# Performance work log

Hardware: AMD Instinct MI355X
Metric: run time of the kernel (lower is better)

## Reference

```python
import jax, jax.numpy as jnp
import numpy as np
import math

IN_C = 1024
OUT_C = 1024
HEADS = 16
GROUPS = 4

def grouped_linear(src, weight, bias):
    # src: [..., in_c]; weight: [g, in_c//g, out_c//g]; bias: [out_c]
    g, icg, ocg = weight.shape
    lead = src.shape[:-1]
    s = src.reshape(*lead, g, icg)
    out = jnp.einsum('...gi,gio->...go', s, weight)
    out = out.reshape(*lead, g * ocg)
    return out + bias

def restricted_softmax(src, margin=0.0):
    src_max = jnp.maximum(jnp.max(src, axis=-1, keepdims=True), 0.0)
    out = jnp.exp(src - src_max)
    return out / (jnp.sum(out, axis=-1, keepdims=True) + jnp.exp(margin - src_max))

def setup_inputs() -> dict:
    key = jax.random.key(0)
    ks = jax.random.split(key, 9)
    B, S = 2, 2048
    icg, ocg = IN_C // GROUPS, OUT_C // GROUPS
    scale = 1.0 / math.sqrt(icg)
    return {
        'query': jax.random.normal(ks[0], (B, S, IN_C), jnp.float32),
        'key': jax.random.normal(ks[1], (B, S, IN_C), jnp.float32),
        'value': jax.random.normal(ks[2], (B, S, IN_C), jnp.float32),
        'wq': jax.random.uniform(ks[3], (GROUPS, icg, ocg), jnp.float32, -scale, scale),
        'wk': jax.random.uniform(ks[4], (GROUPS, icg, ocg), jnp.float32, -scale, scale),
        'wv': jax.random.uniform(ks[5], (GROUPS, icg, ocg), jnp.float32, -scale, scale),
        'bq': jax.random.uniform(ks[6], (OUT_C,), jnp.float32, -scale, scale),
        'bk': jax.random.uniform(ks[7], (OUT_C,), jnp.float32, -scale, scale),
        'bv': jax.random.uniform(ks[8], (OUT_C,), jnp.float32, -scale, scale),
    }

def reference(query, key, value, wq, wk, wv, bq, bk, bv):
    q = grouped_linear(query, wq, bq)   # [B,S,OUT_C]
    k = grouped_linear(key, wk, bk)
    v = grouped_linear(value, wv, bv)
    B, Sq, _ = q.shape
    Sk = k.shape[-2]
    d = OUT_C // HEADS
    q = q.reshape(B, Sq, HEADS, d).transpose(0, 2, 1, 3)  # [B,H,Sq,d]
    k = k.reshape(B, Sk, HEADS, d).transpose(0, 2, 1, 3)
    v = v.reshape(B, Sk, HEADS, d).transpose(0, 2, 1, 3)
    score = jnp.einsum('bhqd,bhkd->bhqk', q, k) / math.sqrt(d)
    attn = restricted_softmax(score)
    out = jnp.einsum('bhqk,bhkd->bhqd', attn, v)
    out = out.transpose(0, 2, 1, 3).reshape(B, Sq, OUT_C)
    return out
```

## Files before the change

kernel.cpp:

```cpp
#include <hip/hip_runtime.h>
#include <hip/hip_bf16.h>

#define BB 2
#define SS 2048
#define CC 1024
#define HH 16
#define DDIM 64
#define NROWS (BB*SS)

#define QSC 0.18033688011112042f

typedef __attribute__((ext_vector_type(8))) short bf16x8;
typedef __attribute__((ext_vector_type(4))) float f32x4;

__device__ __forceinline__ f32x4 mfma16(bf16x8 a, bf16x8 b, f32x4 c) {
    return __builtin_amdgcn_mfma_f32_16x16x32_bf16(a, b, c, 0, 0, 0);
}

__global__ __launch_bounds__(256) void prep_wt(
    const float* __restrict__ wq, const float* __restrict__ wk,
    const float* __restrict__ wv, __hip_bfloat16* __restrict__ wt)
{
    const float* w = blockIdx.z == 0 ? wq : blockIdx.z == 1 ? wk : wv;
    const int g  = blockIdx.y;
    const int kt = blockIdx.x >> 2;
    const int nt = blockIdx.x & 3;
    __shared__ __hip_bfloat16 Ls[64][72];
    const int t = threadIdx.x;
    #pragma unroll
    for (int j = 0; j < 4; ++j) {
        int f4 = t + j*256;
        int row = f4 >> 4, n0 = (f4 & 15) * 4;
        float4 f = *(const float4*)&w[(size_t)g*65536 + (size_t)(kt*64+row)*256
                                      + nt*64 + n0];
        Ls[n0+0][row] = __float2bfloat16(f.x);
        Ls[n0+1][row] = __float2bfloat16(f.y);
        Ls[n0+2][row] = __float2bfloat16(f.z);
        Ls[n0+3][row] = __float2bfloat16(f.w);
    }
    __syncthreads();
    #pragma unroll
    for (int j = 0; j < 2; ++j) {
        int u = t + j*256;
        int nr = u >> 3, k8 = (u & 7) * 8;
        *(uint4*)&wt[((size_t)(blockIdx.z*4 + g)*256 + nt*64 + nr)*256
                     + kt*64 + k8] = *(const uint4*)&Ls[nr][k8];
    }
}

__global__ __launch_bounds__(256, 3) void proj_mfma(
    const float* __restrict__ qin, const float* __restrict__ kin,
    const float* __restrict__ vin,
    const __hip_bfloat16* __restrict__ wt,
    const float* __restrict__ bq, const float* __restrict__ bk,
    const float* __restrict__ bv,
    __hip_bfloat16* __restrict__ qs, __hip_bfloat16* __restrict__ ks_,
    __hip_bfloat16* __restrict__ vs)
{
    const int z = blockIdx.z;
    const float* src; const float* bias;
    if (z == 0)      { src = qin; bias = bq; }
    else if (z == 1) { src = kin; bias = bk; }
    else             { src = vin; bias = bv; }

    const int hp   = blockIdx.y;
    const int g    = hp >> 1;
    const int col0 = (hp & 1) * 128;
    const int row0 = blockIdx.x * 128;
    const int b    = row0 >> 11;
    const int s0   = row0 & 2047;

    __shared__ char smem[36864];
    auto As = (__hip_bfloat16 (*)[72])smem;
    auto Ws = (__hip_bfloat16 (*)[72])(smem + 18432);

    const int t    = threadIdx.x;
    const int wid  = t >> 6;
    const int lane = t & 63;
    const int l16  = lane & 15;
    const int quad = lane >> 4;

    f32x4 acc[2][8];
    #pragma unroll
    for (int mt = 0; mt < 2; ++mt)
        #pragma unroll
        for (int nt = 0; nt < 8; ++nt) acc[mt][nt] = (f32x4){0.f,0.f,0.f,0.f};

    const __hip_bfloat16* wtz = wt + (size_t)(z*4 + g)*65536;

    for (int kt = 0; kt < 4; ++kt) {
        __syncthreads();
        #pragma unroll
        for (int j = 0; j < 8; ++j) {
            int idx = t + j*256;
            int row = idx >> 4, c4 = (idx & 15) * 4;
            float4 f = *(const float4*)&src[(size_t)(row0 + row)*CC + g*256
                                            + kt*64 + c4];
            union { __hip_bfloat16 hh[4]; uint2 u; } pk;
            pk.hh[0] = __float2bfloat16(f.x); pk.hh[1] = __float2bfloat16(f.y);
            pk.hh[2] = __float2bfloat16(f.z); pk.hh[3] = __float2bfloat16(f.w);
            *(uint2*)&As[row][c4] = pk.u;
        }
        #pragma unroll
        for (int j = 0; j < 4; ++j) {
            int idx = t + j*256;
            int n = idx >> 3, k8 = (idx & 7) * 8;
            *(uint4*)&Ws[n][k8] =
                *(const uint4*)&wtz[(size_t)(col0 + n)*256 + kt*64 + k8];
        }
        __syncthreads();
        #pragma unroll
        for (int kss = 0; kss < 2; ++kss) {
            bf16x8 af[2], wf[8];
            #pragma unroll
            for (int mt = 0; mt < 2; ++mt)
                af[mt] = *(const bf16x8*)&As[wid*32 + mt*16 + l16][kss*32 + quad*8];
            #pragma unroll
            for (int nt = 0; nt < 8; ++nt)
                wf[nt] = *(const bf16x8*)&Ws[nt*16 + l16][kss*32 + quad*8];
            #pragma unroll
            for (int mt = 0; mt < 2; ++mt)
                #pragma unroll
                for (int nt = 0; nt < 8; ++nt)
                    acc[mt][nt] = mfma16(af[mt], wf[nt], acc[mt][nt]);
        }
    }

    float bval[8];
    #pragma unroll
    for (int nt = 0; nt < 8; ++nt) bval[nt] = bias[g*256 + col0 + nt*16 + l16];

    __syncthreads();

    if (z < 2) {
        const float scale = (z == 0) ? QSC : 1.0f;
        auto Ot = (__hip_bfloat16 (*)[136])smem;
        #pragma unroll
        for (int mt = 0; mt < 2; ++mt)
            #pragma unroll
            for (int nt = 0; nt < 8; ++nt)
                #pragma unroll
                for (int r = 0; r < 4; ++r)
                    Ot[wid*32 + mt*16 + quad*4 + r][nt*16 + l16] =
                        __float2bfloat16((acc[mt][nt][r] + bval[nt]) * scale);
        __syncthreads();
        __hip_bfloat16* base = (z == 0) ? qs : ks_;
        #pragma unroll
        for (int j = 0; j < 8; ++j) {
            int f = wid + j*4;
            int hl = f >> 4, t16l = (f >> 1) & 7, kcs = f & 1;
            uint4 v = *(const uint4*)&Ot[t16l*16 + l16][hl*64 + kcs*32 + quad*8];
            int h = hp*2 + hl;
            int t16g = (s0 >> 4) + t16l;
            *(uint4*)&base[((size_t)(b*HH + h) << 17)
                           + ((size_t)(t16g*2 + kcs) << 9) + lane*8] = v;
        }
    } else {
        auto Vl = (__hip_bfloat16 (*)[136])smem;
        #pragma unroll
        for (int mt = 0; mt < 2; ++mt)
            #pragma unroll
            for (int nt = 0; nt < 8; ++nt) {
                union { __hip_bfloat16 hh[4]; uint2 u; } pk;
                #pragma unroll
                for (int r = 0; r < 4; ++r)
                    pk.hh[r] = __float2bfloat16(acc[mt][nt][r] + bval[nt]);
                *(uint2*)&Vl[nt*16 + l16][wid*32 + mt*16 + quad*4] = pk.u;
            }
        __syncthreads();
        const int kc0 = s0 >> 5;
        #pragma unroll
        for (int j = 0; j < 8; ++j) {
            int f = wid + j*4;
            int hl = f >> 4, dt = (f >> 2) & 3, kcl = f & 3;
            uint4 v = *(const uint4*)&Vl[hl*64 + dt*16 + l16][kcl*32 + quad*8];
            int h = hp*2 + hl;
            *(uint4*)&vs[((size_t)(b*HH + h) << 17)
                         + ((size_t)(dt*64 + kc0 + kcl) << 9) + lane*8] = v;
        }
    }
}

__global__ __launch_bounds__(256, 2) void attn_mfma(
    const __hip_bfloat16* __restrict__ qs, const __hip_bfloat16* __restrict__ ks_,
    const __hip_bfloat16* __restrict__ vs, float* __restrict__ out)
{
    const int d   = blockIdx.x;
    const int xcd = d & 7;
    const int s   = d >> 3;
    const int qt  = s & 31;
    const int bh  = (s >> 5) * 8 + xcd;
    const int h   = bh & 15;
    const int b   = bh >> 4;

    __shared__ char smem[37376];
    auto Ps = (__hip_bfloat16 (*)[64][72])smem;
    auto Ub = (float (*)[64][68])smem;
    float* Lb = (float*)(smem + 36864);

    const int t    = threadIdx.x;
    const int wid  = t >> 6;
    const int lane = t & 63;
    const int l16  = lane & 15;
    const int quad = lane >> 4;

    const __hip_bfloat16* qb = qs  + ((size_t)bh << 17);
    const __hip_bfloat16* kb = ks_ + ((size_t)bh << 17);
    const __hip_bfloat16* vb = vs  + ((size_t)bh << 17);

    const bf16x8 onesv = (bf16x8){16256,16256,16256,16256,
                                  16256,16256,16256,16256};

    bf16x8 qf[4][2];
    #pragma unroll
    for (int mt = 0; mt < 4; ++mt)
        #pragma unroll
        for (int kss = 0; kss < 2; ++kss)
            qf[mt][kss] = *(const bf16x8*)(qb +
                ((size_t)((qt*4 + mt)*2 + kss) << 9) + lane*8);

    f32x4 O[4][4];
    f32x4 Lfrag[4];
    #pragma unroll
    for (int mt = 0; mt < 4; ++mt) {
        Lfrag[mt] = (f32x4){0.f,0.f,0.f,0.f};
        #pragma unroll
        for (int dt = 0; dt < 4; ++dt) O[mt][dt] = (f32x4){0.f,0.f,0.f,0.f};
    }

    bf16x8 kf[4][2];
    #pragma unroll
    for (int nt = 0; nt < 4; ++nt)
        #pragma unroll
        for (int kss = 0; kss < 2; ++kss)
            kf[nt][kss] = *(const bf16x8*)(kb +
                ((size_t)((wid*32 + nt)*2 + kss) << 9) + lane*8);

    for (int kt = 0; kt < 8; ++kt) {
        bf16x8 vf[4][2];
        #pragma unroll
        for (int dt = 0; dt < 4; ++dt)
            #pragma unroll
            for (int kss = 0; kss < 2; ++kss)
                vf[dt][kss] = *(const bf16x8*)(vb +
                    ((size_t)(dt*64 + wid*16 + kt*2 + kss) << 9) + lane*8);

        #pragma unroll
        for (int nt = 0; nt < 4; ++nt) {
            f32x4 st[4];
            #pragma unroll
            for (int mt = 0; mt < 4; ++mt) {
                f32x4 z = (f32x4){0.f,0.f,0.f,0.f};
                z = mfma16(kf[nt][0], qf[mt][0], z);
                st[mt] = mfma16(kf[nt][1], qf[mt][1], z);
            }
            #pragma unroll
            for (int mt = 0; mt < 4; ++mt) {
                float2 e0, e1;
                e0.x = __builtin_amdgcn_exp2f(st[mt][0]);
                e0.y = __builtin_amdgcn_exp2f(st[mt][1]);
                e1.x = __builtin_amdgcn_exp2f(st[mt][2]);
                e1.y = __builtin_amdgcn_exp2f(st[mt][3]);
                union { __hip_bfloat162 h2[2]; uint2 u; } pk;
                pk.h2[0] = __float22bfloat162_rn(e0);
                pk.h2[1] = __float22bfloat162_rn(e1);
                *(uint2*)&Ps[wid][mt*16 + l16][nt*16 + quad*4] = pk.u;
            }
        }

        if (kt + 1 < 8) {
            #pragma unroll
            for (int nt = 0; nt < 4; ++nt)
                #pragma unroll
                for (int kss = 0; kss < 2; ++kss)
                    kf[nt][kss] = *(const bf16x8*)(kb +
                        ((size_t)((wid*32 + (kt+1)*4 + nt)*2 + kss) << 9) + lane*8);
        }

        #pragma unroll
        for (int kss = 0; kss < 2; ++kss) {
            bf16x8 pf[4];
            #pragma unroll
            for (int mt = 0; mt < 4; ++mt)
                pf[mt] = *(const bf16x8*)&Ps[wid][mt*16 + l16][kss*32 + quad*8];
            #pragma unroll
            for (int mt = 0; mt < 4; ++mt) {
                Lfrag[mt] = mfma16(onesv, pf[mt], Lfrag[mt]);
                #pragma unroll
                for (int dt = 0; dt < 4; ++dt)
                    O[mt][dt] = mfma16(vf[dt][kss], pf[mt], O[mt][dt]);
            }
        }
    }

    __syncthreads();
    if (wid & 1) {
        const int half = wid >> 1;
        #pragma unroll
        for (int mt = 0; mt < 4; ++mt) {
            if (quad == 0) Lb[half*64 + mt*16 + l16] = Lfrag[mt][0];
            #pragma unroll
            for (int dt = 0; dt < 4; ++dt) {
                float4 u4;
                u4.x = O[mt][dt][0]; u4.y = O[mt][dt][1];
                u4.z = O[mt][dt][2]; u4.w = O[mt][dt][3];
                *(float4*)&Ub[half][mt*16 + l16][dt*16 + quad*4] = u4;
            }
        }
    }
    __syncthreads();
    if (!(wid & 1)) {
        const int half = wid >> 1;
        #pragma unroll
        for (int mt = 0; mt < 4; ++mt) {
            Lfrag[mt][0] += Lb[half*64 + mt*16 + l16];
            #pragma unroll
            for (int dt = 0; dt < 4; ++dt) {
                float4 u4 = *(const float4*)&Ub[half][mt*16 + l16][dt*16 + quad*4];
                O[mt][dt][0] += u4.x; O[mt][dt][1] += u4.y;
                O[mt][dt][2] += u4.z; O[mt][dt][3] += u4.w;
            }
        }
    }
    if (wid == 2) {
        #pragma unroll
        for (int mt = 0; mt < 4; ++mt) {
            if (quad == 0) Lb[64 + mt*16 + l16] = Lfrag[mt][0];
            #pragma unroll
            for (int dt = 0; dt < 4; ++dt) {
                float4 u4;
                u4.x = O[mt][dt][0]; u4.y = O[mt][dt][1];
                u4.z = O[mt][dt][2]; u4.w = O[mt][dt][3];
                *(float4*)&Ub[1][mt*16 + l16][dt*16 + quad*4] = u4;
            }
        }
    }
    __syncthreads();
    if (wid == 0) {
        #pragma unroll
        for (int mt = 0; mt < 4; ++mt) {
            const float inv = 1.0f /
                (1.0f + Lfrag[mt][0] + Lb[64 + mt*16 + l16]);
            const size_t row = (size_t)b*SS + qt*64 + mt*16 + l16;
            #pragma unroll
            for (int dt = 0; dt < 4; ++dt) {
                float4 u4 = *(const float4*)&Ub[1][mt*16 + l16][dt*16 + quad*4];
                float4 o4;
                o4.x = (O[mt][dt][0] + u4.x) * inv;
                o4.y = (O[mt][dt][1] + u4.y) * inv;
                o4.z = (O[mt][dt][2] + u4.z) * inv;
                o4.w = (O[mt][dt][3] + u4.w) * inv;
                *(float4*)&out[row*CC + h*DDIM + dt*16 + quad*4] = o4;
            }
        }
    }
}

extern "C" void kernel_launch(void* const* d_in, const int* in_sizes, int n_in,
                              void* d_out, int out_size, void* d_ws, size_t ws_size,
                              hipStream_t stream) {
    (void)in_sizes; (void)n_in; (void)out_size; (void)ws_size;
    const float* qin = (const float*)d_in[0];
    const float* kin = (const float*)d_in[1];
    const float* vin = (const float*)d_in[2];
    const float* wq  = (const float*)d_in[3];
    const float* wk  = (const float*)d_in[4];
    const float* wv  = (const float*)d_in[5];
    const float* bq  = (const float*)d_in[6];
    const float* bk  = (const float*)d_in[7];
    const float* bv  = (const float*)d_in[8];

    char* w0 = (char*)d_ws;
    __hip_bfloat16* qs = (__hip_bfloat16*)(w0);
    __hip_bfloat16* ks = (__hip_bfloat16*)(w0 + 8388608);
    __hip_bfloat16* vs = (__hip_bfloat16*)(w0 + 16777216);
    __hip_bfloat16* wt = (__hip_bfloat16*)(w0 + 25165824);
    float* out = (float*)d_out;

    prep_wt<<<dim3(16, 4, 3), 256, 0, stream>>>(wq, wk, wv, wt);
    proj_mfma<<<dim3(32, 8, 3), 256, 0, stream>>>(
        qin, kin, vin, wt, bq, bk, bv, qs, ks, vs);
    attn_mfma<<<dim3(1024, 1, 1), 256, 0, stream>>>(qs, ks, vs, out);
}
```

Measured before the change: 162.4 us.

## Prepack weights in MFMA fragment order and double-buffer activation tiles

The weight-prep kernel now writes bf16 weights pre-arranged in MFMA fragment order, so the projection kernel reads B fragments straight from global memory and no longer stages weights in shared memory. Activation tiles are double-buffered in LDS, with the next K-tile's float loads issued as register prefetch before the current tile's MFMAs, which removes one barrier per iteration. Launch bounds drop the occupancy hint from 3 to 2 to leave room for the extra prefetch registers. The cost is lower occupancy and per-wave global loads for weights, which depend on cache hits.

```diff
diff --git a/kernel.cpp b/kernel.cpp
--- a/kernel.cpp
+++ b/kernel.cpp
@@ -22,9 +22,9 @@
     const float* __restrict__ wv, __hip_bfloat16* __restrict__ wt)
 {
     const float* w = blockIdx.z == 0 ? wq : blockIdx.z == 1 ? wk : wv;
-    const int g  = blockIdx.y;
-    const int kt = blockIdx.x >> 2;
-    const int nt = blockIdx.x & 3;
+    const int g   = blockIdx.y;
+    const int kt  = blockIdx.x >> 2;
+    const int ntb = blockIdx.x & 3;
     __shared__ __hip_bfloat16 Ls[64][72];
     const int t = threadIdx.x;
     #pragma unroll
@@ -32,23 +32,30 @@
         int f4 = t + j*256;
         int row = f4 >> 4, n0 = (f4 & 15) * 4;
         float4 f = *(const float4*)&w[(size_t)g*65536 + (size_t)(kt*64+row)*256
-                                      + nt*64 + n0];
+                                      + ntb*64 + n0];
         Ls[n0+0][row] = __float2bfloat16(f.x);
         Ls[n0+1][row] = __float2bfloat16(f.y);
         Ls[n0+2][row] = __float2bfloat16(f.z);
         Ls[n0+3][row] = __float2bfloat16(f.w);
     }
     __syncthreads();
+    const int zg = blockIdx.z*4 + g;
+    const int ch = ntb >> 1;
     #pragma unroll
     for (int j = 0; j < 2; ++j) {
-        int u = t + j*256;
-        int nr = u >> 3, k8 = (u & 7) * 8;
-        *(uint4*)&wt[((size_t)(blockIdx.z*4 + g)*256 + nt*64 + nr)*256
-                     + kt*64 + k8] = *(const uint4*)&Ls[nr][k8];
+        int u    = t + j*256;
+        int n16g = u >> 7;
+        int kss  = (u >> 6) & 1;
+        int lane = u & 63;
+        int l16  = lane & 15, quad = lane >> 4;
+        int nt   = (ntb & 1)*4 + n16g;
+        size_t frag = (((size_t)(zg*2 + ch)*4 + kt)*2 + kss)*8 + nt;
+        *(uint4*)&wt[frag*512 + lane*8] =
+            *(const uint4*)&Ls[n16g*16 + l16][kss*32 + quad*8];
     }
 }
 
-__global__ __launch_bounds__(256, 3) void proj_mfma(
+__global__ __launch_bounds__(256, 2) void proj_mfma(
     const float* __restrict__ qin, const float* __restrict__ kin,
     const float* __restrict__ vin,
     const __hip_bfloat16* __restrict__ wt,
@@ -65,14 +72,14 @@
 
     const int hp   = blockIdx.y;
     const int g    = hp >> 1;
-    const int col0 = (hp & 1) * 128;
+    const int ch   = hp & 1;
+    const int col0 = ch * 128;
     const int row0 = blockIdx.x * 128;
     const int b    = row0 >> 11;
     const int s0   = row0 & 2047;
 
     __shared__ char smem[36864];
-    auto As = (__hip_bfloat16 (*)[72])smem;
-    auto Ws = (__hip_bfloat16 (*)[72])(smem + 18432);
+    auto As = (__hip_bfloat16 (*)[128][72])smem;
 
     const int t    = threadIdx.x;
     const int wid  = t >> 6;
@@ -86,51 +93,68 @@
         #pragma unroll
         for (int nt = 0; nt < 8; ++nt) acc[mt][nt] = (f32x4){0.f,0.f,0.f,0.f};
 
-    const __hip_bfloat16* wtz = wt + (size_t)(z*4 + g)*65536;
+    const __hip_bfloat16* wfb = wt + ((size_t)((z*4 + g)*2 + ch) << 15);
+
+    #pragma unroll
+    for (int j = 0; j < 8; ++j) {
+        int idx = t + j*256;
+        int row = idx >> 4, c4 = (idx & 15) * 4;
+        float4 f = *(const float4*)&src[(size_t)(row0 + row)*CC + g*256 + c4];
+        union { __hip_bfloat16 hh[4]; uint2 u; } pk;
+        pk.hh[0] = __float2bfloat16(f.x); pk.hh[1] = __float2bfloat16(f.y);
+        pk.hh[2] = __float2bfloat16(f.z); pk.hh[3] = __float2bfloat16(f.w);
+        *(uint2*)&As[0][row][c4] = pk.u;
+    }
+    __syncthreads();
 
     for (int kt = 0; kt < 4; ++kt) {
-        __syncthreads();
-        #pragma unroll
-        for (int j = 0; j < 8; ++j) {
-            int idx = t + j*256;
-            int row = idx >> 4, c4 = (idx & 15) * 4;
-            float4 f = *(const float4*)&src[(size_t)(row0 + row)*CC + g*256
-                                            + kt*64 + c4];
-            union { __hip_bfloat16 hh[4]; uint2 u; } pk;
-            pk.hh[0] = __float2bfloat16(f.x); pk.hh[1] = __float2bfloat16(f.y);
-            pk.hh[2] = __float2bfloat16(f.z); pk.hh[3] = __float2bfloat16(f.w);
-            *(uint2*)&As[row][c4] = pk.u;
-        }
-        #pragma unroll
-        for (int j = 0; j < 4; ++j) {
-            int idx = t + j*256;
-            int n = idx >> 3, k8 = (idx & 7) * 8;
-            *(uint4*)&Ws[n][k8] =
-                *(const uint4*)&wtz[(size_t)(col0 + n)*256 + kt*64 + k8];
-        }
-        __syncthreads();
+        const int cur = kt & 1;
+        float4 fr[8];
+        if (kt < 3) {
+            #pragma unroll
+            for (int j = 0; j < 8; ++j) {
+                int idx = t + j*256;
+                int row = idx >> 4, c4 = (idx & 15) * 4;
+                fr[j] = *(const float4*)&src[(size_t)(row0 + row)*CC + g*256
+                                             + (kt+1)*64 + c4];
+            }
+        }
         #pragma unroll
         for (int kss = 0; kss < 2; ++kss) {
             bf16x8 af[2], wf[8];
             #pragma unroll
             for (int mt = 0; mt < 2; ++mt)
-                af[mt] = *(const bf16x8*)&As[wid*32 + mt*16 + l16][kss*32 + quad*8];
+                af[mt] = *(const bf16x8*)
+                    &As[cur][wid*32 + mt*16 + l16][kss*32 + quad*8];
             #pragma unroll
             for (int nt = 0; nt < 8; ++nt)
-                wf[nt] = *(const bf16x8*)&Ws[nt*16 + l16][kss*32 + quad*8];
+                wf[nt] = *(const bf16x8*)
+                    (wfb + (((size_t)(kt*2 + kss)*8 + nt) << 9) + lane*8);
             #pragma unroll
             for (int mt = 0; mt < 2; ++mt)
                 #pragma unroll
                 for (int nt = 0; nt < 8; ++nt)
                     acc[mt][nt] = mfma16(af[mt], wf[nt], acc[mt][nt]);
         }
+        if (kt < 3) {
+            #pragma unroll
+            for (int j = 0; j < 8; ++j) {
+                int idx = t + j*256;
+                int row = idx >> 4, c4 = (idx & 15) * 4;
+                union { __hip_bfloat16 hh[4]; uint2 u; } pk;
+                pk.hh[0] = __float2bfloat16(fr[j].x);
+                pk.hh[1] = __float2bfloat16(fr[j].y);
+                pk.hh[2] = __float2bfloat16(fr[j].z);
+                pk.hh[3] = __float2bfloat16(fr[j].w);
+                *(uint2*)&As[cur^1][row][c4] = pk.u;
+            }
+        }
+        __syncthreads();
     }
 
     float bval[8];
     #pragma unroll
     for (int nt = 0; nt < 8; ++nt) bval[nt] = bias[g*256 + col0 + nt*16 + l16];
-
-    __syncthreads();
 
     if (z < 2) {
         const float scale = (z == 0) ? QSC : 1.0f;
```

New measurement: 160.0 us (median of 2 runs). No clear change (-1.5%).
